# Kernel tuning notes

Measured on AMD Instinct MI355X. Metric: run time of the kernel, lower is better.

The kernel has to match this reference:

```python
import jax, jax.numpy as jnp
import numpy as np

L, H, NH, NKV, HD, I, MAXS = 5, 1024, 16, 8, 128, 3072, 16
EPS = 1e-6
THETA = 1000000.0
N_REP = NH // NKV


def rms(x, w, eps=EPS):
    # RMSNorm over last dim (fp32 math as in the torch module)
    return w * (x * jax.lax.rsqrt(jnp.mean(x * x, axis=-1, keepdims=True) + eps))


def rotate_half(v):
    d = v.shape[-1] // 2
    return jnp.concatenate([-v[..., d:], v[..., :d]], axis=-1)


def setup_inputs() -> dict:
    key = jax.random.key(0)
    ks = jax.random.split(key, 20)
    s = 0.02
    inp = {
        'hidden_states': jax.random.normal(ks[0], (1, 1, H), jnp.float32),
        'position_id': jax.random.randint(ks[1], (1,), 0, MAXS, jnp.int64) if jax.config.jax_enable_x64 else jax.random.randint(ks[1], (1,), 0, MAXS).astype(jnp.int32),
        'past_keys': jax.random.normal(ks[2], (L, 1, NKV, MAXS, HD), jnp.float32),
        'past_values': jax.random.normal(ks[3], (L, 1, NKV, MAXS, HD), jnp.float32),
        'w_iln': jnp.ones((L, H), jnp.float32),
        'w_paln': jnp.ones((L, H), jnp.float32),
        'wq': jax.random.normal(ks[4], (L, NH * HD, H), jnp.float32) * s,
        'wk': jax.random.normal(ks[5], (L, NKV * HD, H), jnp.float32) * s,
        'wv': jax.random.normal(ks[6], (L, NKV * HD, H), jnp.float32) * s,
        'wo': jax.random.normal(ks[7], (L, H, NH * HD), jnp.float32) * s,
        'w_qn': jnp.ones((L, HD), jnp.float32),
        'w_kn': jnp.ones((L, HD), jnp.float32),
        'w_gate': jax.random.normal(ks[8], (L, I, H), jnp.float32) * s,
        'w_up': jax.random.normal(ks[9], (L, I, H), jnp.float32) * s,
        'w_down': jax.random.normal(ks[10], (L, H, I), jnp.float32) * s,
        'w_onorm': jnp.ones((H,), jnp.float32),
    }
    return inp


def reference(hidden_states, position_id, past_keys, past_values,
              w_iln, w_paln, wq, wk, wv, wo, w_qn, w_kn,
              w_gate, w_up, w_down, w_onorm):
    pos = position_id[0]
    # RoPE tables at the single decode position
    inv_freq = 1.0 / (THETA ** (jnp.arange(0, HD, 2, dtype=jnp.float32) / HD))  # [HD/2]
    freqs = pos.astype(jnp.float32) * inv_freq
    cos = jnp.concatenate([jnp.cos(freqs)] * 2)  # [HD]
    sin = jnp.concatenate([jnp.sin(freqs)] * 2)
    mask = jnp.arange(MAXS) > pos  # [MAXS] future positions masked
    scale = 1.0 / jnp.sqrt(jnp.float32(HD))

    x = hidden_states[0, 0]  # [H]

    def layer(x, xs):
        pk, pv, wi, wp, q_, k_, v_, o_, qn, kn, g_, u_, d_ = xs
        h = rms(x, wi)
        q = (q_ @ h).reshape(NH, HD)
        k_new = rms((k_ @ h).reshape(NKV, HD), kn)
        v_new = (v_ @ h).reshape(NKV, HD)
        q = rms(q, qn)
        q = q * cos + rotate_half(q) * sin
        k_new = k_new * cos + rotate_half(k_new) * sin
        # write new K/V at pos into the fixed-size cache
        kc = pk[0].at[:, pos, :].set(k_new)  # [NKV, MAXS, HD]
        vc = pv[0].at[:, pos, :].set(v_new)
        # GQA: repeat each kv head N_REP times (contiguous, matching torch expand)
        ke = jnp.repeat(kc, N_REP, axis=0)  # [NH, MAXS, HD]
        ve = jnp.repeat(vc, N_REP, axis=0)
        scores = jnp.einsum('hd,hkd->hk', q, ke) * scale
        scores = jnp.where(mask[None, :], -jnp.inf, scores)
        p = jax.nn.softmax(scores, axis=-1)
        attn = jnp.einsum('hk,hkd->hd', p, ve).reshape(NH * HD)
        x = x + o_ @ attn
        h = rms(x, wp)
        x = x + d_ @ (jax.nn.silu(g_ @ h) * (u_ @ h))
        return x, (kc[None], vc[None])

    xs = (past_keys, past_values, w_iln, w_paln, wq, wk, wv, wo,
          w_qn, w_kn, w_gate, w_up, w_down)
    x, (pks, pvs) = jax.lax.scan(layer, x, xs)
    out = rms(x, w_onorm)[None, None, :]  # [1,1,H]
    return out, pks, pvs


if __name__ == '__main__':
    o = reference(**setup_inputs())
    print(o[0].shape, o[1].shape, o[2].shape)
```

## Files before the change

kernel.cpp:

```cpp
#include <hip/hip_runtime.h>
#include <hip/hip_bf16.h>
#include <math.h>

typedef __hip_bfloat16 bf16;
typedef unsigned long long ull;

#define L_    5
#define H_    1024
#define NH_   16
#define NKV_  8
#define HD_   128
#define I_    3072
#define MAXS_ 16
#define EPS_  1e-6f
#define KVE_  (L_ * NKV_ * MAXS_ * HD_)
#define GRID_ 512
#define BAR_OFF 10496

static __device__ __forceinline__ float bl(unsigned u){ return __uint_as_float(u << 16); }
static __device__ __forceinline__ float bh(unsigned u){ return __uint_as_float(u & 0xffff0000u); }
static __device__ __forceinline__ float b2f(bf16 v){ return __bfloat162float(v); }

static __device__ __forceinline__ float wred(float v){
#pragma unroll
    for (int o = 32; o; o >>= 1) v += __shfl_xor(v, o, 64);
    return v;
}

static __device__ __forceinline__ float dot8(uint4 u, float4 a, float4 b){
    return bl(u.x)*a.x + bh(u.x)*a.y + bl(u.y)*a.z + bh(u.y)*a.w
         + bl(u.z)*b.x + bh(u.z)*b.y + bl(u.w)*b.z + bh(u.w)*b.w;
}

static __device__ __forceinline__ float rms_inv(float sumsq, float n){
    float a = sumsq / n + EPS_;
    float y = rsqrtf(a);
    y = y * (1.5f - 0.5f * a * y * y);
    return y;
}

static __device__ __forceinline__ float gld(const float* p){
    return __hip_atomic_load((float*)p, __ATOMIC_RELAXED, __HIP_MEMORY_SCOPE_AGENT);
}
static __device__ __forceinline__ void gst(float* p, float v){
    __hip_atomic_store(p, v, __ATOMIC_RELAXED, __HIP_MEMORY_SCOPE_AGENT);
}
static __device__ __forceinline__ void gst8(ull* p, ull v){
    __hip_atomic_store(p, v, __ATOMIC_RELAXED, __HIP_MEMORY_SCOPE_AGENT);
}

static __device__ __forceinline__ float ld1(const void* p, size_t i, bool b16){
    return b16 ? b2f(((const bf16*)p)[i]) : ((const float*)p)[i];
}
static __device__ __forceinline__ void st1(void* p, size_t i, float v, bool b16){
    if (b16) ((bf16*)p)[i] = __float2bfloat16(v);
    else     ((float*)p)[i] = v;
}

static __device__ __forceinline__ float rowdot(const void* w, size_t off, int n,
                                               const float* hs, bool b16, int lane){
    float acc = 0.f;
    if (b16) {
        const uint4* wp = (const uint4*)((const ushort*)w + off);
#pragma unroll 6
        for (int c = 0; c < n / 512; c++) {
            uint4 u = wp[c * 64 + lane];
            const float4* h4 = (const float4*)&hs[c * 512 + lane * 8];
            acc += dot8(u, h4[0], h4[1]);
        }
    } else {
        const float4* wp = (const float4*)((const float*)w + off);
#pragma unroll 12
        for (int c = 0; c < n / 256; c++) {
            float4 u = wp[c * 64 + lane];
            float4 h = *(const float4*)&hs[c * 256 + lane * 4];
            acc += u.x * h.x + u.y * h.y + u.z * h.z + u.w * h.w;
        }
    }
    return acc;
}

static __device__ __forceinline__ void gsync(unsigned* bar, unsigned p, int gid){
    __syncthreads();
    if (threadIdx.x == 0) {
        unsigned* sub    = bar + ((gid >> 5) * 32);
        unsigned* master = bar + 512;
        unsigned* gen    = bar + 544;
        asm volatile("s_waitcnt vmcnt(0)" ::: "memory");
        unsigned a = __hip_atomic_fetch_add(sub, 1u, __ATOMIC_RELAXED, __HIP_MEMORY_SCOPE_AGENT) + 1u;
        if (a == 32u * p) {
            unsigned m = __hip_atomic_fetch_add(master, 1u, __ATOMIC_RELAXED, __HIP_MEMORY_SCOPE_AGENT) + 1u;
            if (m == 16u * p)
                __hip_atomic_store(gen, p, __ATOMIC_RELAXED, __HIP_MEMORY_SCOPE_AGENT);
        }
        while (__hip_atomic_load(gen, __ATOMIC_RELAXED, __HIP_MEMORY_SCOPE_AGENT) < p)
            __builtin_amdgcn_s_sleep(8);
        asm volatile("" ::: "memory");
    }
    __syncthreads();
}

__global__ void k_zero(float* __restrict__ ws){
    int t = threadIdx.x;
    if (t < 16) ws[10240 + t] = 0.f;
    unsigned* bar = (unsigned*)(ws + BAR_OFF);
    for (int i = t; i < 576; i += 256) bar[i] = 0u;
}

__global__ __launch_bounds__(256, 2) void k_model(
        const void* __restrict__ hid, const int* __restrict__ pos_p,
        const void* __restrict__ pk,  const void* __restrict__ pv,
        const void* __restrict__ w_iln, const void* __restrict__ w_paln,
        const void* __restrict__ wq,  const void* __restrict__ wk,
        const void* __restrict__ wv,  const void* __restrict__ wo,
        const void* __restrict__ w_qn, const void* __restrict__ w_kn,
        const void* __restrict__ w_gate, const void* __restrict__ w_up,
        const void* __restrict__ w_down, const void* __restrict__ w_onorm,
        float* __restrict__ ws, void* __restrict__ out)
{
    __shared__ float sh[I_];
    __shared__ float red[4];
    __shared__ float s_inv;

    const int gid = blockIdx.x, tid = threadIdx.x;
    const int lane = tid & 63, wid = tid >> 6;
    const bool b16 = (((const ushort*)w_onorm)[0] == 0x3F80);
    int pos = pos_p[0];
    pos = pos < 0 ? 0 : (pos > MAXS_ - 1 ? MAXS_ - 1 : pos);

    float* x    = ws;
    float* qraw = x + 1024;
    float* kraw = qraw + 2048;
    float* vraw = kraw + 1024;
    float* attn = vraw + 1024;
    float* act  = attn + 2048;
    float* ss   = ws + 10240;
    unsigned* bar = (unsigned*)(ws + BAR_OFF);
    unsigned ph = 0;

    {
        const size_t esz = b16 ? 2 : 4;
        const size_t nll = (size_t)KVE_ * esz / 8;
        const ull* sk = (const ull*)pk;
        const ull* sv = (const ull*)pv;
        ull* dk = (ull*)((char*)out + (size_t)H_ * esz);
        ull* dv = dk + nll;
        for (size_t i = (size_t)gid * 256 + tid; i < nll; i += (size_t)GRID_ * 256) {
            gst8(dk + i, sk[i]);
            gst8(dv + i, sv[i]);
        }
        if (gid == 0) {
            float s0 = 0.f;
            for (int j = tid; j < H_; j += 256) {
                float v = ld1(hid, j, b16);
                gst(&x[j], v); s0 += v * v;
            }
            s0 = wred(s0);
            if (lane == 0) red[wid] = s0;
            __syncthreads();
            if (tid == 0) gst(&ss[0], red[0] + red[1] + red[2] + red[3]);
        }
        gsync(bar, ++ph, gid);
    }

    for (int l = 0; l < L_; l++) {
        {
            if (tid == 0) s_inv = rms_inv(gld(&ss[2 * l]), (float)H_);
            __syncthreads();
            float inv = s_inv;
            for (int j = tid; j < H_; j += 256)
                sh[j] = gld(&x[j]) * inv * ld1(w_iln, (size_t)l * H_ + j, b16);
            __syncthreads();
            for (int rr = wid; rr < 8; rr += 4) {
                int r = gid * 8 + rr;
                const void* w; size_t off; float* dst;
                if (r < NH_ * HD_) {
                    w = wq; off = (size_t)l * NH_ * HD_ * H_ + (size_t)r * H_; dst = qraw + r;
                } else if (r < NH_ * HD_ + NKV_ * HD_) {
                    int rk = r - NH_ * HD_;
                    w = wk; off = (size_t)l * NKV_ * HD_ * H_ + (size_t)rk * H_; dst = kraw + rk;
                } else {
                    int rv = r - NH_ * HD_ - NKV_ * HD_;
                    w = wv; off = (size_t)l * NKV_ * HD_ * H_ + (size_t)rv * H_; dst = vraw + rv;
                }
                float acc = wred(rowdot(w, off, H_, sh, b16, lane));
                if (lane == 0) gst(dst, acc);
            }
            gsync(bar, ++ph, gid);
        }

        if (gid < NH_ && wid == 0) {
            int hh = gid, g = hh >> 1;
            float fr = (float)pos * exp2f(-(float)lane * 0.31143075889569023f);
            float c = cosf(fr), s = sinf(fr);

            float q0 = gld(&qraw[hh * HD_ + lane]), q1 = gld(&qraw[hh * HD_ + 64 + lane]);
            float qi = rms_inv(wred(q0 * q0 + q1 * q1), (float)HD_);
            q0 *= qi * ld1(w_qn, (size_t)l * HD_ + lane, b16);
            q1 *= qi * ld1(w_qn, (size_t)l * HD_ + 64 + lane, b16);
            float q0r = q0 * c - q1 * s, q1r = q1 * c + q0 * s;

            float k0 = gld(&kraw[g * HD_ + lane]), k1 = gld(&kraw[g * HD_ + 64 + lane]);
            float ki = rms_inv(wred(k0 * k0 + k1 * k1), (float)HD_);
            k0 *= ki * ld1(w_kn, (size_t)l * HD_ + lane, b16);
            k1 *= ki * ld1(w_kn, (size_t)l * HD_ + 64 + lane, b16);
            float k0r = k0 * c - k1 * s, k1r = k1 * c + k0 * s;

            float v0 = gld(&vraw[g * HD_ + lane]), v1 = gld(&vraw[g * HD_ + 64 + lane]);

            size_t kco = H_ + (size_t)l * NKV_ * MAXS_ * HD_ + (size_t)g * MAXS_ * HD_;
            size_t vco = kco + KVE_;
            const float scale = 0.08838834764831845f;

            float sc[MAXS_];
            float m = -3.0e38f;
#pragma unroll
            for (int t = 0; t < MAXS_; t++) {
                float d = (t == pos)
                    ? (q0r * k0r + q1r * k1r)
                    : (q0r * ld1(out, kco + t * HD_ + lane, b16)
                     + q1r * ld1(out, kco + t * HD_ + 64 + lane, b16));
                d = wred(d) * scale;
                sc[t] = d;
                if (t <= pos) m = fmaxf(m, d);
            }
            float se = 0.f;
#pragma unroll
            for (int t = 0; t < MAXS_; t++) {
                float e = (t <= pos) ? expf(sc[t] - m) : 0.0f;
                sc[t] = e; se += e;
            }
            float rinv = 1.0f / se;
            float a0 = 0.f, a1 = 0.f;
#pragma unroll
            for (int t = 0; t < MAXS_; t++) {
                float pt = sc[t] * rinv;
                if (t == pos) { a0 += pt * v0; a1 += pt * v1; }
                else {
                    a0 += pt * ld1(out, vco + t * HD_ + lane, b16);
                    a1 += pt * ld1(out, vco + t * HD_ + 64 + lane, b16);
                }
            }
            gst(&attn[hh * HD_ + lane],      a0);
            gst(&attn[hh * HD_ + 64 + lane], a1);
            if ((hh & 1) == 0) {
                st1(out, kco + pos * HD_ + lane,      k0r, b16);
                st1(out, kco + pos * HD_ + 64 + lane, k1r, b16);
                st1(out, vco + pos * HD_ + lane,      v0,  b16);
                st1(out, vco + pos * HD_ + 64 + lane, v1,  b16);
            }
        }
        gsync(bar, ++ph, gid);

        if (gid < 256) {
            for (int j = tid; j < NH_ * HD_; j += 256) sh[j] = gld(&attn[j]);
            __syncthreads();
            int r = gid * 4 + wid;
            size_t off = (size_t)l * H_ * NH_ * HD_ + (size_t)r * NH_ * HD_;
            float acc = wred(rowdot(wo, off, NH_ * HD_, sh, b16, lane));
            if (lane == 0) {
                float xn = gld(&x[r]) + acc;
                gst(&x[r], xn);
                red[wid] = xn * xn;
            }
            __syncthreads();
            if (tid == 0) atomicAdd(&ss[2 * l + 1], red[0] + red[1] + red[2] + red[3]);
        }
        gsync(bar, ++ph, gid);

        {
            if (tid == 0) s_inv = rms_inv(gld(&ss[2 * l + 1]), (float)H_);
            __syncthreads();
            float inv = s_inv;
            for (int j = tid; j < H_; j += 256)
                sh[j] = gld(&x[j]) * inv * ld1(w_paln, (size_t)l * H_ + j, b16);
            __syncthreads();
            for (int pp = wid; pp < 6; pp += 4) {
                int i = gid * 6 + pp;
                size_t off = (size_t)l * I_ * H_ + (size_t)i * H_;
                float ag = wred(rowdot(w_gate, off, H_, sh, b16, lane));
                float au = wred(rowdot(w_up,   off, H_, sh, b16, lane));
                if (lane == 0) {
                    float sig = 1.0f / (1.0f + expf(-ag));
                    gst(&act[i], ag * sig * au);
                }
            }
            gsync(bar, ++ph, gid);
        }

        if (gid < 256) {
            for (int j = tid; j < I_; j += 256) sh[j] = gld(&act[j]);
            __syncthreads();
            int r = gid * 4 + wid;
            size_t off = (size_t)l * H_ * I_ + (size_t)r * I_;
            float acc = wred(rowdot(w_down, off, I_, sh, b16, lane));
            if (lane == 0) {
                float xn = gld(&x[r]) + acc;
                gst(&x[r], xn);
                red[wid] = xn * xn;
            }
            __syncthreads();
            if (tid == 0) atomicAdd(&ss[2 * l + 2], red[0] + red[1] + red[2] + red[3]);
        }
        gsync(bar, ++ph, gid);
    }

    if (gid == 0) {
        if (tid == 0) s_inv = rms_inv(gld(&ss[10]), (float)H_);
        __syncthreads();
        float inv = s_inv;
        for (int j = tid; j < H_; j += 256)
            st1(out, j, gld(&x[j]) * inv * ld1(w_onorm, j, b16), b16);
    }
}

extern "C" void kernel_launch(void* const* d_in, const int* in_sizes, int n_in,
                              void* d_out, int out_size, void* d_ws, size_t ws_size,
                              hipStream_t stream) {
    const void* hid     = d_in[0];
    const int*  pos     = (const int*)d_in[1];
    const void* pk      = d_in[2];
    const void* pv      = d_in[3];
    const void* w_iln   = d_in[4];
    const void* w_paln  = d_in[5];
    const void* wq      = d_in[6];
    const void* wk      = d_in[7];
    const void* wv      = d_in[8];
    const void* wo      = d_in[9];
    const void* w_qn    = d_in[10];
    const void* w_kn    = d_in[11];
    const void* w_gate  = d_in[12];
    const void* w_up    = d_in[13];
    const void* w_down  = d_in[14];
    const void* w_onorm = d_in[15];
    float* ws = (float*)d_ws;

    k_zero<<<1, 256, 0, stream>>>(ws);
    k_model<<<GRID_, 256, 0, stream>>>(hid, pos, pk, pv, w_iln, w_paln,
                                       wq, wk, wv, wo, w_qn, w_kn,
                                       w_gate, w_up, w_down, w_onorm,
                                       ws, d_out);
}
```

Before: 498.9 us.

## Replace grid barriers with per-stage counters and prefetch weights into registers

Replaces the hierarchical grid-wide barrier with monotonically increasing per-stage counters (qkv, attention, o-proj, gate/up, down), so each block waits only on the producers it actually depends on. Weight rows for the next matmul stages, and the next layer's QKV rows, are loaded into registers before the wait, which overlaps memory latency with synchronisation. The kernel is also templated on the bf16/fp32 element type to drop runtime branches. The cost is much higher register pressure from holding the prefetched rows, which may spill or lower occupancy, plus tighter spin-wait polling.

```diff
diff --git a/kernel.cpp b/kernel.cpp
--- a/kernel.cpp
+++ b/kernel.cpp
@@ -15,11 +15,11 @@
 #define EPS_  1e-6f
 #define KVE_  (L_ * NKV_ * MAXS_ * HD_)
 #define GRID_ 512
+#define SS_OFF  10240
 #define BAR_OFF 10496
 
 static __device__ __forceinline__ float bl(unsigned u){ return __uint_as_float(u << 16); }
 static __device__ __forceinline__ float bh(unsigned u){ return __uint_as_float(u & 0xffff0000u); }
-static __device__ __forceinline__ float b2f(bf16 v){ return __bfloat162float(v); }
 
 static __device__ __forceinline__ float wred(float v){
 #pragma unroll
@@ -49,62 +49,358 @@
     __hip_atomic_store(p, v, __ATOMIC_RELAXED, __HIP_MEMORY_SCOPE_AGENT);
 }
 
+static __device__ __forceinline__ void waitc(unsigned* c, unsigned tgt){
+    while (__hip_atomic_load(c, __ATOMIC_RELAXED, __HIP_MEMORY_SCOPE_AGENT) < tgt)
+        __builtin_amdgcn_s_sleep(1);
+}
+static __device__ __forceinline__ void incc(unsigned* c){
+    __hip_atomic_fetch_add(c, 1u, __ATOMIC_RELAXED, __HIP_MEMORY_SCOPE_AGENT);
+}
+
 static __device__ __forceinline__ float ld1(const void* p, size_t i, bool b16){
-    return b16 ? b2f(((const bf16*)p)[i]) : ((const float*)p)[i];
+    return b16 ? __uint_as_float((unsigned)((const ushort*)p)[i] << 16) : ((const float*)p)[i];
 }
 static __device__ __forceinline__ void st1(void* p, size_t i, float v, bool b16){
     if (b16) ((bf16*)p)[i] = __float2bfloat16(v);
     else     ((float*)p)[i] = v;
 }
 
-static __device__ __forceinline__ float rowdot(const void* w, size_t off, int n,
-                                               const float* hs, bool b16, int lane){
-    float acc = 0.f;
-    if (b16) {
-        const uint4* wp = (const uint4*)((const ushort*)w + off);
-#pragma unroll 6
-        for (int c = 0; c < n / 512; c++) {
-            uint4 u = wp[c * 64 + lane];
-            const float4* h4 = (const float4*)&hs[c * 512 + lane * 8];
-            acc += dot8(u, h4[0], h4[1]);
-        }
+template<bool B16> struct ET { typedef float T;
+    static __device__ __forceinline__ float tof(T v){ return v; } };
+template<> struct ET<true> { typedef ushort T;
+    static __device__ __forceinline__ float tof(T v){ return __uint_as_float((unsigned)v << 16); } };
+
+template<bool B16, int N> struct Pf {
+    static constexpr int C = B16 ? (N / 512) : (N / 256);
+    uint4 v[C];
+    __device__ __forceinline__ void load(const void* w, size_t off, int lane){
+        const uint4* wp = B16 ? (const uint4*)((const ushort*)w + off)
+                              : (const uint4*)((const float*)w + off);
+#pragma unroll
+        for (int c = 0; c < C; c++) v[c] = wp[c * 64 + lane];
+    }
+    __device__ __forceinline__ float dot(const float* hs, int lane) const {
+        float acc = 0.f;
+        if (B16) {
+#pragma unroll
+            for (int c = 0; c < C; c++) {
+                const float4* h4 = (const float4*)&hs[c * 512 + lane * 8];
+                acc += dot8(v[c], h4[0], h4[1]);
+            }
+        } else {
+#pragma unroll
+            for (int c = 0; c < C; c++) {
+                float4 f = *(const float4*)&v[c];
+                const float4* h = (const float4*)&hs[c * 256 + lane * 4];
+                acc += f.x*h->x + f.y*h->y + f.z*h->z + f.w*h->w;
+            }
+        }
+        return acc;
+    }
+};
+
+static __device__ __forceinline__ void q_addr(int r, int l,
+        const void* wq, const void* wk, const void* wv,
+        float* qraw, float* kraw, float* vraw,
+        const void*& w, size_t& off, float*& dst){
+    if (r < NH_ * HD_) {
+        w = wq; off = (size_t)l * NH_ * HD_ * H_ + (size_t)r * H_; dst = qraw + r;
+    } else if (r < NH_ * HD_ + NKV_ * HD_) {
+        int rk = r - NH_ * HD_;
+        w = wk; off = (size_t)l * NKV_ * HD_ * H_ + (size_t)rk * H_; dst = kraw + rk;
     } else {
-        const float4* wp = (const float4*)((const float*)w + off);
-#pragma unroll 12
-        for (int c = 0; c < n / 256; c++) {
-            float4 u = wp[c * 64 + lane];
-            float4 h = *(const float4*)&hs[c * 256 + lane * 4];
-            acc += u.x * h.x + u.y * h.y + u.z * h.z + u.w * h.w;
-        }
-    }
-    return acc;
-}
-
-static __device__ __forceinline__ void gsync(unsigned* bar, unsigned p, int gid){
-    __syncthreads();
-    if (threadIdx.x == 0) {
-        unsigned* sub    = bar + ((gid >> 5) * 32);
-        unsigned* master = bar + 512;
-        unsigned* gen    = bar + 544;
-        asm volatile("s_waitcnt vmcnt(0)" ::: "memory");
-        unsigned a = __hip_atomic_fetch_add(sub, 1u, __ATOMIC_RELAXED, __HIP_MEMORY_SCOPE_AGENT) + 1u;
-        if (a == 32u * p) {
-            unsigned m = __hip_atomic_fetch_add(master, 1u, __ATOMIC_RELAXED, __HIP_MEMORY_SCOPE_AGENT) + 1u;
-            if (m == 16u * p)
-                __hip_atomic_store(gen, p, __ATOMIC_RELAXED, __HIP_MEMORY_SCOPE_AGENT);
-        }
-        while (__hip_atomic_load(gen, __ATOMIC_RELAXED, __HIP_MEMORY_SCOPE_AGENT) < p)
-            __builtin_amdgcn_s_sleep(8);
-        asm volatile("" ::: "memory");
-    }
-    __syncthreads();
+        int rv = r - NH_ * HD_ - NKV_ * HD_;
+        w = wv; off = (size_t)l * NKV_ * HD_ * H_ + (size_t)rv * H_; dst = vraw + rv;
+    }
 }
 
 __global__ void k_zero(float* __restrict__ ws){
     int t = threadIdx.x;
-    if (t < 16) ws[10240 + t] = 0.f;
+    if (t < 16) ws[SS_OFF + t] = 0.f;
     unsigned* bar = (unsigned*)(ws + BAR_OFF);
-    for (int i = t; i < 576; i += 256) bar[i] = 0u;
+    for (int i = t; i < 192; i += 256) bar[i] = 0u;
+}
+
+template<bool B16>
+static __device__ __forceinline__ void run(
+        const void* hid, int pos,
+        const void* pk, const void* pv,
+        const void* w_iln, const void* w_paln,
+        const void* wq, const void* wk, const void* wv, const void* wo,
+        const void* w_qn, const void* w_kn,
+        const void* w_gate, const void* w_up, const void* w_down,
+        const void* w_onorm,
+        float* ws, void* out,
+        float* sh, float* red, float* s_inv_p)
+{
+    typedef typename ET<B16>::T KVT;
+    const int gid = blockIdx.x, tid = threadIdx.x;
+    const int lane = tid & 63, wid = tid >> 6;
+
+    float* x    = ws;
+    float* qraw = ws + 1024;
+    float* kraw = ws + 3072;
+    float* vraw = ws + 4096;
+    float* attn = ws + 5120;
+    float* act  = ws + 7168;
+    float* ss   = ws + SS_OFF;
+    unsigned* bar  = (unsigned*)(ws + BAR_OFF);
+    unsigned* icnt = bar;
+    unsigned* qcnt = bar + 32;
+    unsigned* acnt = bar + 64;
+    unsigned* ocnt = bar + 96;
+    unsigned* gcnt = bar + 128;
+    unsigned* dcnt = bar + 160;
+
+    Pf<B16, H_> qA, qB;
+    {
+        const void* w; size_t off; float* dst;
+        q_addr(gid * 8 + wid, 0, wq, wk, wv, qraw, kraw, vraw, w, off, dst);
+        qA.load(w, off, lane);
+        q_addr(gid * 8 + wid + 4, 0, wq, wk, wv, qraw, kraw, vraw, w, off, dst);
+        qB.load(w, off, lane);
+    }
+    asm volatile("" ::: "memory");
+
+    {
+        const size_t esz = B16 ? 2 : 4;
+        const size_t nll = (size_t)KVE_ * esz / 8;
+        const ull* sk = (const ull*)pk;
+        const ull* sv = (const ull*)pv;
+        ull* dk = (ull*)((char*)out + (size_t)H_ * esz);
+        ull* dv = dk + nll;
+        for (size_t i = (size_t)gid * 256 + tid; i < nll; i += (size_t)GRID_ * 256) {
+            gst8(dk + i, sk[i]);
+            gst8(dv + i, sv[i]);
+        }
+        if (gid == 0) {
+            float s0 = 0.f;
+            for (int j = tid; j < H_; j += 256) {
+                float v = ld1(hid, j, B16);
+                gst(&x[j], v); s0 += v * v;
+            }
+            s0 = wred(s0);
+            if (lane == 0) red[wid] = s0;
+            __syncthreads();
+            if (tid == 0) gst(&ss[0], red[0] + red[1] + red[2] + red[3]);
+        }
+        __syncthreads();
+        if (tid == 0) incc(icnt);
+    }
+
+    for (int l = 0; l < L_; ++l) {
+        if (tid == 0) {
+            if (l == 0) waitc(icnt, (unsigned)GRID_);
+            else        waitc(dcnt, 256u * l);
+            *s_inv_p = rms_inv(gld(&ss[2 * l]), (float)H_);
+        }
+        __syncthreads();
+        {
+            float inv = *s_inv_p;
+            for (int j = tid; j < H_; j += 256)
+                sh[j] = gld(&x[j]) * inv * ld1(w_iln, (size_t)l * H_ + j, B16);
+        }
+        __syncthreads();
+        {
+            const void* w; size_t off; float* dst;
+            q_addr(gid * 8 + wid, l, wq, wk, wv, qraw, kraw, vraw, w, off, dst);
+            float acc = wred(qA.dot(sh, lane));
+            if (lane == 0) gst(dst, acc);
+            q_addr(gid * 8 + wid + 4, l, wq, wk, wv, qraw, kraw, vraw, w, off, dst);
+            acc = wred(qB.dot(sh, lane));
+            if (lane == 0) gst(dst, acc);
+        }
+        __syncthreads();
+        if (tid == 0) incc(qcnt);
+
+        KVT a_k0[MAXS_], a_k1[MAXS_], a_v0[MAXS_], a_v1[MAXS_];
+        size_t kco = 0, vco = 0;
+        if (gid < NH_ && wid == 0) {
+            int g = gid >> 1;
+            kco = H_ + (size_t)l * NKV_ * MAXS_ * HD_ + (size_t)g * MAXS_ * HD_;
+            vco = kco + KVE_;
+            const KVT* ob = (const KVT*)out;
+#pragma unroll
+            for (int t = 0; t < MAXS_; t++) {
+                a_k0[t] = ob[kco + t * HD_ + lane];
+                a_k1[t] = ob[kco + t * HD_ + 64 + lane];
+                a_v0[t] = ob[vco + t * HD_ + lane];
+                a_v1[t] = ob[vco + t * HD_ + 64 + lane];
+            }
+        }
+        Pf<B16, NH_ * HD_> oRow;
+        if (gid < 256)
+            oRow.load(wo, (size_t)l * H_ * NH_ * HD_ + (size_t)(gid * 4 + wid) * NH_ * HD_, lane);
+        Pf<B16, H_> gA, gU, hA, hU;
+        {
+            int i0 = gid * 6 + wid;
+            size_t offg = (size_t)l * I_ * H_ + (size_t)i0 * H_;
+            gA.load(w_gate, offg, lane);
+            gU.load(w_up,   offg, lane);
+            if (wid < 2) {
+                size_t offh = (size_t)l * I_ * H_ + (size_t)(i0 + 4) * H_;
+                hA.load(w_gate, offh, lane);
+                hU.load(w_up,   offh, lane);
+            }
+        }
+        asm volatile("" ::: "memory");
+
+        if (gid < NH_ && wid == 0) {
+            waitc(qcnt, 512u * (l + 1));
+            int hh = gid;
+            int g  = hh >> 1;
+            float fr = (float)pos * exp2f(-(float)lane * 0.31143075889569023f);
+            float c = cosf(fr), s = sinf(fr);
+
+            float q0 = gld(&qraw[hh * HD_ + lane]), q1 = gld(&qraw[hh * HD_ + 64 + lane]);
+            float qi = rms_inv(wred(q0 * q0 + q1 * q1), (float)HD_);
+            q0 *= qi * ld1(w_qn, (size_t)l * HD_ + lane, B16);
+            q1 *= qi * ld1(w_qn, (size_t)l * HD_ + 64 + lane, B16);
+            float q0r = q0 * c - q1 * s, q1r = q1 * c + q0 * s;
+
+            float k0 = gld(&kraw[g * HD_ + lane]), k1 = gld(&kraw[g * HD_ + 64 + lane]);
+            float ki = rms_inv(wred(k0 * k0 + k1 * k1), (float)HD_);
+            k0 *= ki * ld1(w_kn, (size_t)l * HD_ + lane, B16);
+            k1 *= ki * ld1(w_kn, (size_t)l * HD_ + 64 + lane, B16);
+            float k0r = k0 * c - k1 * s, k1r = k1 * c + k0 * s;
+
+            float v0 = gld(&vraw[g * HD_ + lane]), v1 = gld(&vraw[g * HD_ + 64 + lane]);
+
+            const float scale = 0.08838834764831845f;
+            float scb[MAXS_];
+            float m = -3.0e38f;
+#pragma unroll
+            for (int t = 0; t < MAXS_; t++) {
+                float d = (t == pos)
+                    ? (q0r * k0r + q1r * k1r)
+                    : (q0r * ET<B16>::tof(a_k0[t]) + q1r * ET<B16>::tof(a_k1[t]));
+                d = wred(d) * scale;
+                scb[t] = d;
+                if (t <= pos) m = fmaxf(m, d);
+            }
+            float se = 0.f;
+#pragma unroll
+            for (int t = 0; t < MAXS_; t++) {
+                float e = (t <= pos) ? expf(scb[t] - m) : 0.0f;
+                scb[t] = e; se += e;
+            }
+            float rinv = 1.0f / se;
+            float a0 = 0.f, a1 = 0.f;
+#pragma unroll
+            for (int t = 0; t < MAXS_; t++) {
+                float pt = scb[t] * rinv;
+                if (t == pos) { a0 += pt * v0; a1 += pt * v1; }
+                else {
+                    a0 += pt * ET<B16>::tof(a_v0[t]);
+                    a1 += pt * ET<B16>::tof(a_v1[t]);
+                }
+            }
+            gst(&attn[hh * HD_ + lane],      a0);
+            gst(&attn[hh * HD_ + 64 + lane], a1);
+            if ((hh & 1) == 0) {
+                st1(out, kco + pos * HD_ + lane,      k0r, B16);
+                st1(out, kco + pos * HD_ + 64 + lane, k1r, B16);
+                st1(out, vco + pos * HD_ + lane,      v0,  B16);
+                st1(out, vco + pos * HD_ + 64 + lane, v1,  B16);
+            }
+            asm volatile("s_waitcnt vmcnt(0)" ::: "memory");
+            if (lane == 0) incc(acnt);
+        }
+
+        if (gid < 256) {
+            if (tid == 0) waitc(acnt, 16u * (l + 1));
+            __syncthreads();
+            for (int j = tid; j < NH_ * HD_; j += 256) sh[j] = gld(&attn[j]);
+            __syncthreads();
+            int r = gid * 4 + wid;
+            float acc = wred(oRow.dot(sh, lane));
+            if (lane == 0) {
+                float xn = gld(&x[r]) + acc;
+                gst(&x[r], xn);
+                red[wid] = xn * xn;
+            }
+            __syncthreads();
+            if (tid == 0) {
+                atomicAdd(&ss[2 * l + 1], red[0] + red[1] + red[2] + red[3]);
+                asm volatile("s_waitcnt vmcnt(0)" ::: "memory");
+                incc(ocnt);
+            }
+        }
+
+        if (tid == 0) {
+            waitc(ocnt, 256u * (l + 1));
+            *s_inv_p = rms_inv(gld(&ss[2 * l + 1]), (float)H_);
+        }
+        __syncthreads();
+        {
+            float inv = *s_inv_p;
+            for (int j = tid; j < H_; j += 256)
+                sh[j] = gld(&x[j]) * inv * ld1(w_paln, (size_t)l * H_ + j, B16);
+        }
+        __syncthreads();
+        {
+            int i0 = gid * 6 + wid;
+            float ag = wred(gA.dot(sh, lane));
+            float au = wred(gU.dot(sh, lane));
+            if (lane == 0) {
+                float sig = 1.0f / (1.0f + expf(-ag));
+                gst(&act[i0], ag * sig * au);
+            }
+            if (wid < 2) {
+                ag = wred(hA.dot(sh, lane));
+                au = wred(hU.dot(sh, lane));
+                if (lane == 0) {
+                    float sig = 1.0f / (1.0f + expf(-ag));
+                    gst(&act[i0 + 4], ag * sig * au);
+                }
+            }
+        }
+        __syncthreads();
+        if (tid == 0) incc(gcnt);
+
+        Pf<B16, I_> dRow;
+        if (gid < 256)
+            dRow.load(w_down, (size_t)l * H_ * I_ + (size_t)(gid * 4 + wid) * I_, lane);
+        if (l + 1 < L_) {
+            const void* w; size_t off; float* dst;
+            q_addr(gid * 8 + wid, l + 1, wq, wk, wv, qraw, kraw, vraw, w, off, dst);
+            qA.load(w, off, lane);
+            q_addr(gid * 8 + wid + 4, l + 1, wq, wk, wv, qraw, kraw, vraw, w, off, dst);
+            qB.load(w, off, lane);
+        }
+        asm volatile("" ::: "memory");
+
+        if (gid < 256) {
+            if (tid == 0) waitc(gcnt, 512u * (l + 1));
+            __syncthreads();
+            for (int j = tid; j < I_; j += 256) sh[j] = gld(&act[j]);
+            __syncthreads();
+            int r = gid * 4 + wid;
+            float acc = wred(dRow.dot(sh, lane));
+            if (lane == 0) {
+                float xn = gld(&x[r]) + acc;
+                gst(&x[r], xn);
+                red[wid] = xn * xn;
+            }
+            __syncthreads();
+            if (tid == 0) {
+                atomicAdd(&ss[2 * l + 2], red[0] + red[1] + red[2] + red[3]);
+                asm volatile("s_waitcnt vmcnt(0)" ::: "memory");
+                incc(dcnt);
+            }
+        }
+    }
+
+    if (gid == 0) {
+        if (tid == 0) {
+            waitc(dcnt, 256u * L_);
+            *s_inv_p = rms_inv(gld(&ss[2 * L_]), (float)H_);
+        }
+        __syncthreads();
+        float inv = *s_inv_p;
+        for (int j = tid; j < H_; j += 256)
+            st1(out, j, gld(&x[j]) * inv * ld1(w_onorm, j, B16), B16);
+    }
 }
 
 __global__ __launch_bounds__(256, 2) void k_model(
@@ -122,196 +418,18 @@
     __shared__ float red[4];
     __shared__ float s_inv;
 
-    const int gid = blockIdx.x, tid = threadIdx.x;
-    const int lane = tid & 63, wid = tid >> 6;
     const bool b16 = (((const ushort*)w_onorm)[0] == 0x3F80);
     int pos = pos_p[0];
     pos = pos < 0 ? 0 : (pos > MAXS_ - 1 ? MAXS_ - 1 : pos);
 
-    float* x    = ws;
-    float* qraw = x + 1024;
-    float* kraw = qraw + 2048;
-    float* vraw = kraw + 1024;
-    float* attn = vraw + 1024;
-    float* act  = attn + 2048;
-    float* ss   = ws + 10240;
-    unsigned* bar = (unsigned*)(ws + BAR_OFF);
-    unsigned ph = 0;
-
-    {
-        const size_t esz = b16 ? 2 : 4;
-        const size_t nll = (size_t)KVE_ * esz / 8;
-        const ull* sk = (const ull*)pk;
-        const ull* sv = (const ull*)pv;
-        ull* dk = (ull*)((char*)out + (size_t)H_ * esz);
-        ull* dv = dk + nll;
-        for (size_t i = (size_t)gid * 256 + tid; i < nll; i += (size_t)GRID_ * 256) {
-            gst8(dk + i, sk[i]);
-            gst8(dv + i, sv[i]);
-        }
-        if (gid == 0) {
-            float s0 = 0.f;
-            for (int j = tid; j < H_; j += 256) {
-                float v = ld1(hid, j, b16);
-                gst(&x[j], v); s0 += v * v;
-            }
-            s0 = wred(s0);
-            if (lane == 0) red[wid] = s0;
-            __syncthreads();
-            if (tid == 0) gst(&ss[0], red[0] + red[1] + red[2] + red[3]);
-        }
-        gsync(bar, ++ph, gid);
-    }
-
-    for (int l = 0; l < L_; l++) {
-        {
-            if (tid == 0) s_inv = rms_inv(gld(&ss[2 * l]), (float)H_);
-            __syncthreads();
-            float inv = s_inv;
-            for (int j = tid; j < H_; j += 256)
-                sh[j] = gld(&x[j]) * inv * ld1(w_iln, (size_t)l * H_ + j, b16);
-            __syncthreads();
-            for (int rr = wid; rr < 8; rr += 4) {
-                int r = gid * 8 + rr;
-                const void* w; size_t off; float* dst;
-                if (r < NH_ * HD_) {
-                    w = wq; off = (size_t)l * NH_ * HD_ * H_ + (size_t)r * H_; dst = qraw + r;
-                } else if (r < NH_ * HD_ + NKV_ * HD_) {
-                    int rk = r - NH_ * HD_;
-                    w = wk; off = (size_t)l * NKV_ * HD_ * H_ + (size_t)rk * H_; dst = kraw + rk;
-                } else {
-                    int rv = r - NH_ * HD_ - NKV_ * HD_;
-                    w = wv; off = (size_t)l * NKV_ * HD_ * H_ + (size_t)rv * H_; dst = vraw + rv;
-                }
-                float acc = wred(rowdot(w, off, H_, sh, b16, lane));
-                if (lane == 0) gst(dst, acc);
-            }
-            gsync(bar, ++ph, gid);
-        }
-
-        if (gid < NH_ && wid == 0) {
-            int hh = gid, g = hh >> 1;
-            float fr = (float)pos * exp2f(-(float)lane * 0.31143075889569023f);
-            float c = cosf(fr), s = sinf(fr);
-
-            float q0 = gld(&qraw[hh * HD_ + lane]), q1 = gld(&qraw[hh * HD_ + 64 + lane]);
-            float qi = rms_inv(wred(q0 * q0 + q1 * q1), (float)HD_);
-            q0 *= qi * ld1(w_qn, (size_t)l * HD_ + lane, b16);
-            q1 *= qi * ld1(w_qn, (size_t)l * HD_ + 64 + lane, b16);
-            float q0r = q0 * c - q1 * s, q1r = q1 * c + q0 * s;
-
-            float k0 = gld(&kraw[g * HD_ + lane]), k1 = gld(&kraw[g * HD_ + 64 + lane]);
-            float ki = rms_inv(wred(k0 * k0 + k1 * k1), (float)HD_);
-            k0 *= ki * ld1(w_kn, (size_t)l * HD_ + lane, b16);
-            k1 *= ki * ld1(w_kn, (size_t)l * HD_ + 64 + lane, b16);
-            float k0r = k0 * c - k1 * s, k1r = k1 * c + k0 * s;
-
-            float v0 = gld(&vraw[g * HD_ + lane]), v1 = gld(&vraw[g * HD_ + 64 + lane]);
-
-            size_t kco = H_ + (size_t)l * NKV_ * MAXS_ * HD_ + (size_t)g * MAXS_ * HD_;
-            size_t vco = kco + KVE_;
-            const float scale = 0.08838834764831845f;
-
-            float sc[MAXS_];
-            float m = -3.0e38f;
-#pragma unroll
-            for (int t = 0; t < MAXS_; t++) {
-                float d = (t == pos)
-                    ? (q0r * k0r + q1r * k1r)
-                    : (q0r * ld1(out, kco + t * HD_ + lane, b16)
-                     + q1r * ld1(out, kco + t * HD_ + 64 + lane, b16));
-                d = wred(d) * scale;
-                sc[t] = d;
-                if (t <= pos) m = fmaxf(m, d);
-            }
-            float se = 0.f;
-#pragma unroll
-            for (int t = 0; t < MAXS_; t++) {
-                float e = (t <= pos) ? expf(sc[t] - m) : 0.0f;
-                sc[t] = e; se += e;
-            }
-            float rinv = 1.0f / se;
-            float a0 = 0.f, a1 = 0.f;
-#pragma unroll
-            for (int t = 0; t < MAXS_; t++) {
-                float pt = sc[t] * rinv;
-                if (t == pos) { a0 += pt * v0; a1 += pt * v1; }
-                else {
-                    a0 += pt * ld1(out, vco + t * HD_ + lane, b16);
-                    a1 += pt * ld1(out, vco + t * HD_ + 64 + lane, b16);
-                }
-            }
-            gst(&attn[hh * HD_ + lane],      a0);
-            gst(&attn[hh * HD_ + 64 + lane], a1);
-            if ((hh & 1) == 0) {
-                st1(out, kco + pos * HD_ + lane,      k0r, b16);
-                st1(out, kco + pos * HD_ + 64 + lane, k1r, b16);
-                st1(out, vco + pos * HD_ + lane,      v0,  b16);
-                st1(out, vco + pos * HD_ + 64 + lane, v1,  b16);
-            }
-        }
-        gsync(bar, ++ph, gid);
-
-        if (gid < 256) {
-            for (int j = tid; j < NH_ * HD_; j += 256) sh[j] = gld(&attn[j]);
-            __syncthreads();
-            int r = gid * 4 + wid;
-            size_t off = (size_t)l * H_ * NH_ * HD_ + (size_t)r * NH_ * HD_;
-            float acc = wred(rowdot(wo, off, NH_ * HD_, sh, b16, lane));
-            if (lane == 0) {
-                float xn = gld(&x[r]) + acc;
-                gst(&x[r], xn);
-                red[wid] = xn * xn;
-            }
-            __syncthreads();
-            if (tid == 0) atomicAdd(&ss[2 * l + 1], red[0] + red[1] + red[2] + red[3]);
-        }
-        gsync(bar, ++ph, gid);
-
-        {
-            if (tid == 0) s_inv = rms_inv(gld(&ss[2 * l + 1]), (float)H_);
-            __syncthreads();
-            float inv = s_inv;
-            for (int j = tid; j < H_; j += 256)
-                sh[j] = gld(&x[j]) * inv * ld1(w_paln, (size_t)l * H_ + j, b16);
-            __syncthreads();
-            for (int pp = wid; pp < 6; pp += 4) {
-                int i = gid * 6 + pp;
-                size_t off = (size_t)l * I_ * H_ + (size_t)i * H_;
-                float ag = wred(rowdot(w_gate, off, H_, sh, b16, lane));
-                float au = wred(rowdot(w_up,   off, H_, sh, b16, lane));
-                if (lane == 0) {
-                    float sig = 1.0f / (1.0f + expf(-ag));
-                    gst(&act[i], ag * sig * au);
-                }
-            }
-            gsync(bar, ++ph, gid);
-        }
-
-        if (gid < 256) {
-            for (int j = tid; j < I_; j += 256) sh[j] = gld(&act[j]);
-            __syncthreads();
-            int r = gid * 4 + wid;
-            size_t off = (size_t)l * H_ * I_ + (size_t)r * I_;
-            float acc = wred(rowdot(w_down, off, I_, sh, b16, lane));
-            if (lane == 0) {
-                float xn = gld(&x[r]) + acc;
-                gst(&x[r], xn);
-                red[wid] = xn * xn;
-            }
-            __syncthreads();
-            if (tid == 0) atomicAdd(&ss[2 * l + 2], red[0] + red[1] + red[2] + red[3]);
-        }
-        gsync(bar, ++ph, gid);
-    }
-
-    if (gid == 0) {
-        if (tid == 0) s_inv = rms_inv(gld(&ss[10]), (float)H_);
-        __syncthreads();
-        float inv = s_inv;
-        for (int j = tid; j < H_; j += 256)
-            st1(out, j, gld(&x[j]) * inv * ld1(w_onorm, j, b16), b16);
-    }
+    if (b16)
+        run<true>(hid, pos, pk, pv, w_iln, w_paln, wq, wk, wv, wo,
+                  w_qn, w_kn, w_gate, w_up, w_down, w_onorm,
+                  ws, out, sh, red, &s_inv);
+    else
+        run<false>(hid, pos, pk, pv, w_iln, w_paln, wq, wk, wv, wo,
+                   w_qn, w_kn, w_gate, w_up, w_down, w_onorm,
+                   ws, out, sh, red, &s_inv);
 }
 
 extern "C" void kernel_launch(void* const* d_in, const int* in_sizes, int n_in,
```

Measured after the change: 708.6 us. +42.0%, slower.
